# Optimization experiments

Measured on AMD Instinct MI355X. Metric: run time of the kernel, lower is better.

## Reference

```python
import jax, jax.numpy as jnp
import numpy as np

B, S, D, H, DH, DK = 2, 2048, 1024, 16, 64, 64


def setup_inputs() -> dict:
    key = jax.random.key(0)
    ks = jax.random.split(key, 11)
    scale_in = 1.0 / np.sqrt(D)
    return {
        "Q": jax.random.normal(ks[0], (B, S, D), jnp.float32),
        "K": jax.random.normal(ks[1], (B, S, D), jnp.float32),
        "V": jax.random.normal(ks[2], (B, S, D), jnp.float32),
        "Wq": jax.random.normal(ks[3], (H, D, DH), jnp.float32) * scale_in,
        "bq": jax.random.normal(ks[4], (H, DH), jnp.float32) * 0.02,
        "Wk": jax.random.normal(ks[5], (H, D, DH), jnp.float32) * scale_in,
        "bk": jax.random.normal(ks[6], (H, DH), jnp.float32) * 0.02,
        "Wv": jax.random.normal(ks[7], (H, D, DH), jnp.float32) * scale_in,
        "bv": jax.random.normal(ks[8], (H, DH), jnp.float32) * 0.02,
        "Wf": jax.random.normal(ks[9], (D, D), jnp.float32) * scale_in,
        "bf": jax.random.normal(ks[10], (D,), jnp.float32) * 0.02,
    }


def reference(Q, K, V, Wq, bq, Wk, bk, Wv, bv, Wf, bf):
    # Per-head projections, vectorized over the head axis h. [B,H,S,DH]
    Qh = jnp.einsum("bsd,hde->bhse", Q, Wq) + bq[None, :, None, :]
    Kh = jnp.einsum("bsd,hde->bhse", K, Wk) + bk[None, :, None, :]
    Vh = jnp.einsum("bsd,hde->bhse", V, Wv) + bv[None, :, None, :]
    inv_sqrt_dk = jnp.asarray(1.0 / np.sqrt(DK), Qh.dtype)
    # Full attention matrix [B,H,S,S] (faithful to the naive original).
    scores = jnp.einsum("bhse,bhte->bhst", Qh, Kh) * inv_sqrt_dk
    attn = jax.nn.softmax(scores, axis=-1)  # F.softmax default -> last dim
    out = jnp.einsum("bhst,bhte->bhse", attn, Vh)  # [B,H,S,DH]
    # Concat heads on the feature axis: [B,S,H*DH] == [B,S,D]
    out = out.transpose(0, 2, 1, 3).reshape(Q.shape[0], Q.shape[1], -1)
    return out @ Wf + bf
```

## Files before the change

### kernel.cpp

```cpp
#include <hip/hip_runtime.h>

#define DEV __device__ __forceinline__

typedef unsigned short u16;
typedef unsigned int   u32;
typedef __attribute__((ext_vector_type(4)))  float f32x4;
typedef __attribute__((ext_vector_type(8)))  short s16x8;
typedef __attribute__((ext_vector_type(2)))  u32   u32x2;

static constexpr size_t OFF_QBF  = 0;
static constexpr size_t OFF_KBF  = 8388608;
static constexpr size_t OFF_VBF  = 16777216;
static constexpr size_t OFF_WCAT = 25165824;
static constexpr size_t OFF_WFT  = 31457280;
static constexpr size_t OFF_BIAS = 33554432;
static constexpr size_t OFF_QKVH = 33566720;
static constexpr size_t OFF_VT   = 58732544;
static constexpr size_t OFF_OBUF = 67121152;

DEV u16 f2bf(float f) {
  union { float f; u32 u; } a; a.f = f;
  u32 r = a.u + 0x7FFFu + ((a.u >> 16) & 1u);
  return (u16)(r >> 16);
}
DEV u32 f2bf2(float lo, float hi_) {
  return (u32)f2bf(lo) | ((u32)f2bf(hi_) << 16);
}

#if __has_builtin(__builtin_amdgcn_exp2f)
DEV float fast_exp2(float x) { return __builtin_amdgcn_exp2f(x); }
#else
DEV float fast_exp2(float x) { return exp2f(x); }
#endif

DEV f32x4 mfma16(s16x8 a, s16x8 b, f32x4 c) {
  return __builtin_amdgcn_mfma_f32_16x16x32_bf16(a, b, c, 0, 0, 0);
}

DEV void gload_lds16(const void* g, void* l) {
  __builtin_amdgcn_global_load_lds(
      (__attribute__((address_space(1))) void*)g,
      (__attribute__((address_space(3))) void*)l, 16, 0, 0);
}

__global__ __launch_bounds__(256) void prep_all_k(const float* __restrict__ Q,
                                                  const float* __restrict__ K,
                                                  const float* __restrict__ V,
                                                  const float* __restrict__ Wq,
                                                  const float* __restrict__ Wk,
                                                  const float* __restrict__ Wv,
                                                  const float* __restrict__ Wf,
                                                  const float* __restrict__ bq,
                                                  const float* __restrict__ bk,
                                                  const float* __restrict__ bv,
                                                  u16* __restrict__ QKVbf,
                                                  u16* __restrict__ Wcat,
                                                  u16* __restrict__ WfT,
                                                  float* __restrict__ biascat) {
  const int bid = blockIdx.x;
  __shared__ u16 t[64][72];
  if (bid < 12288) {
    size_t idx = (size_t)bid * 256 + threadIdx.x;
    size_t tt  = idx >> 20;
    size_t r   = idx & 1048575;
    const float* src = (tt == 0) ? Q : (tt == 1) ? K : V;
    f32x4 v = *(const f32x4*)(src + r * 4);
    u32x2 o;
    o[0] = f2bf2(v[0], v[1]);
    o[1] = f2bf2(v[2], v[3]);
    *(u32x2*)(QKVbf + idx * 4) = o;
  } else if (bid < 13056) {
    const int q = bid - 12288;
    const int dt = q & 15, h = (q >> 4) & 15, z = q >> 8;
    const float* W = (z == 0) ? Wq : (z == 1) ? Wk : Wv;
#pragma unroll
    for (int p = 0; p < 16; ++p) {
      int idx = threadIdx.x + p * 256;
      int r = idx >> 6, e = idx & 63;
      t[r][e] = f2bf(W[((size_t)h * 1024 + dt * 64 + r) * 64 + e]);
    }
    __syncthreads();
#pragma unroll
    for (int p = 0; p < 16; ++p) {
      int idx = threadIdx.x + p * 256;
      int e = idx >> 6, r = idx & 63;
      Wcat[((size_t)z * 1024 + h * 64 + e) * 1024 + dt * 64 + r] = t[r][e];
    }
  } else if (bid < 13312) {
    const int q = bid - 13056;
    const int dt = q & 15, ft = q >> 4;
#pragma unroll
    for (int p = 0; p < 16; ++p) {
      int idx = threadIdx.x + p * 256;
      int r = idx >> 6, f = idx & 63;
      t[r][f] = f2bf(Wf[(size_t)(dt * 64 + r) * 1024 + ft * 64 + f]);
    }
    __syncthreads();
#pragma unroll
    for (int p = 0; p < 16; ++p) {
      int idx = threadIdx.x + p * 256;
      int f = idx >> 6, r = idx & 63;
      WfT[(size_t)(ft * 64 + f) * 1024 + dt * 64 + r] = t[r][f];
    }
  } else {
    int i = (bid - 13312) * 256 + threadIdx.x;
    if (i < 1024) biascat[i] = bq[i];
    else if (i < 2048) biascat[i] = bk[i - 1024];
    else if (i < 3072) biascat[i] = bv[i - 2048];
  }
}

template <int MODE>
DEV void gemm128(const u16* __restrict__ A, int lda,
                 const u16* __restrict__ B, int ldb,
                 const float* __restrict__ bias,
                 void* __restrict__ Cp, size_t ldc, int K) {
  __shared__ u16 Ash[128 * 32];
  __shared__ u16 Bsh[128 * 32];
  const int tid = threadIdx.x;
  const int lane = tid & 63;
  const int w = tid >> 6;
  const int wr = w >> 1, wc = w & 1;
  const int lr = lane >> 2;
  const int lc = (lane & 3) << 3;
  const int l15 = lane & 15, lg = lane >> 4;

  f32x4 acc[4][4];
#pragma unroll
  for (int i = 0; i < 4; ++i)
#pragma unroll
    for (int j = 0; j < 4; ++j) acc[i][j] = f32x4{0.f, 0.f, 0.f, 0.f};

  for (int kt = 0; kt < K; kt += 32) {
    if (kt) __syncthreads();
#pragma unroll
    for (int j = 0; j < 2; ++j) {
      const u16* ga = A + (size_t)(w * 32 + j * 16 + lr) * lda + kt + lc;
      gload_lds16(ga, (char*)Ash + (w * 2 + j) * 1024);
      const u16* gb = B + (size_t)(w * 32 + j * 16 + lr) * ldb + kt + lc;
      gload_lds16(gb, (char*)Bsh + (w * 2 + j) * 1024);
    }
    __syncthreads();
    s16x8 af[4], bv_[4];
#pragma unroll
    for (int i = 0; i < 4; ++i) {
      af[i]  = *(const s16x8*)&Ash[(wr * 64 + i * 16 + l15) * 32 + lg * 8];
      bv_[i] = *(const s16x8*)&Bsh[(wc * 64 + i * 16 + l15) * 32 + lg * 8];
    }
#pragma unroll
    for (int mf = 0; mf < 4; ++mf)
#pragma unroll
      for (int nf = 0; nf < 4; ++nf)
        acc[mf][nf] = mfma16(af[mf], bv_[nf], acc[mf][nf]);
  }
#pragma unroll
  for (int nf = 0; nf < 4; ++nf) {
    const int nn = wc * 64 + nf * 16 + l15;
    const float bvv = bias[nn];
#pragma unroll
    for (int mf = 0; mf < 4; ++mf) {
      if (MODE == 2) {
        const int mm0 = wr * 64 + mf * 16 + lg * 4;
        u32x2 d;
        d[0] = f2bf2(acc[mf][nf][0] + bvv, acc[mf][nf][1] + bvv);
        d[1] = f2bf2(acc[mf][nf][2] + bvv, acc[mf][nf][3] + bvv);
        *(u32x2*)((u16*)Cp + (size_t)nn * ldc + mm0) = d;
      } else {
#pragma unroll
        for (int j = 0; j < 4; ++j) {
          const int mm = wr * 64 + mf * 16 + lg * 4 + j;
          float v = acc[mf][nf][j] + bvv;
          if (MODE == 1) ((u16*)Cp)[(size_t)mm * ldc + nn] = f2bf(v);
          else           ((float*)Cp)[(size_t)mm * ldc + nn] = v;
        }
      }
    }
  }
}

__global__ __launch_bounds__(256) void proj_gemm_k(const u16* __restrict__ Qb,
                                                   const u16* __restrict__ Kb,
                                                   const u16* __restrict__ Vb,
                                                   const u16* __restrict__ Wcat,
                                                   const float* __restrict__ biascat,
                                                   u16* __restrict__ QKVh,
                                                   u16* __restrict__ Vt) {
  const int z = blockIdx.z;
  const u16* A = (z == 0) ? Qb : (z == 1) ? Kb : Vb;
  const int m0 = blockIdx.y * 128;
  const int nl = blockIdx.x * 128;
  if (z == 2) {
    gemm128<2>(A + (size_t)m0 * 1024, 1024,
               Wcat + (size_t)(2 * 1024 + nl) * 1024, 1024,
               biascat + 2 * 1024 + nl,
               Vt + (size_t)nl * 4096 + m0, 4096, 1024);
  } else {
    gemm128<1>(A + (size_t)m0 * 1024, 1024,
               Wcat + (size_t)(z * 1024 + nl) * 1024, 1024,
               biascat + z * 1024 + nl,
               QKVh + (size_t)m0 * 3072 + z * 1024 + nl, 3072, 1024);
  }
}

__global__ __launch_bounds__(256) void final_gemm_k(const u16* __restrict__ Obuf,
                                                    const u16* __restrict__ WfT,
                                                    const float* __restrict__ bf,
                                                    float* __restrict__ out) {
  const int m0 = blockIdx.y * 128;
  const int n0 = blockIdx.x * 128;
  gemm128<0>(Obuf + (size_t)m0 * 1024, 1024,
             WfT + (size_t)n0 * 1024, 1024,
             bf + n0,
             out + (size_t)m0 * 1024 + n0, 1024, 1024);
}

__global__ __launch_bounds__(512) void attn8_k(const u16* __restrict__ QKVh,
                                               const u16* __restrict__ Vt,
                                               u16* __restrict__ Obuf) {
  const int id = blockIdx.x;
  const int virt = (id & 7) * 64 + (id >> 3);
  const int qb = virt & 15;
  const int hb = virt >> 4;
  const int h = hb & 15, b = hb >> 4;

  const int tid = threadIdx.x, lane = tid & 63, w = tid >> 6;
  const int l15 = lane & 15, lg = lane >> 4;

  __shared__ u16 Ksh[64 * 64];
  __shared__ u16 Vsh[64 * 64];
  __shared__ u16 Psh[8][16 * 64];

  const size_t rowQ = (size_t)(b * 2048 + qb * 128);
  const u16* Qbase = QKVh + rowQ * 3072 + h * 64;
  const u16* Kbase = QKVh + (size_t)(b * 2048) * 3072 + 1024 + h * 64;
  const u16* Vbase = Vt + (size_t)(h * 64) * 4096 + b * 2048;

  s16x8 aq[2];
#pragma unroll
  for (int kf = 0; kf < 2; ++kf)
    aq[kf] = *(const s16x8*)(Qbase + (size_t)(w * 16 + l15) * 3072 + kf * 32 + lg * 8);

  f32x4 accO[4];
  f32x4 lacc = f32x4{0.f, 0.f, 0.f, 0.f};
#pragma unroll
  for (int nf = 0; nf < 4; ++nf) accO[nf] = f32x4{0.f, 0.f, 0.f, 0.f};

  const float CSC = 0.18033688011112042f;
  const float M2 = 12.0f;
  const s16x8 ONESV = {0x3F80, 0x3F80, 0x3F80, 0x3F80,
                       0x3F80, 0x3F80, 0x3F80, 0x3F80};

  const int sr = tid >> 3, ch = tid & 7;
  const int sswz = (sr & 7) << 4;
  const u16* Kg = Kbase + (size_t)sr * 3072 + ch * 8;
  const u16* Vg = Vbase + (size_t)sr * 4096 + ch * 8;

  s16x8 kreg = *(const s16x8*)Kg;
  s16x8 vreg = *(const s16x8*)Vg;
  Kg += (size_t)64 * 3072;
  Vg += 64;

  for (int kt = 0; kt < 32; ++kt) {
    if (kt) __syncthreads();
    *(s16x8*)((char*)Ksh + sr * 128 + ((ch * 16) ^ sswz)) = kreg;
    *(s16x8*)((char*)Vsh + sr * 128 + ((ch * 16) ^ sswz)) = vreg;
    __syncthreads();

    if (kt < 31) {
      kreg = *(const s16x8*)Kg;
      vreg = *(const s16x8*)Vg;
      Kg += (size_t)64 * 3072;
      Vg += 64;
    }

    f32x4 sc[4];
#pragma unroll
    for (int nf = 0; nf < 4; ++nf) sc[nf] = f32x4{0.f, 0.f, 0.f, 0.f};
#pragma unroll
    for (int kf = 0; kf < 2; ++kf) {
      s16x8 kb[4];
#pragma unroll
      for (int nf = 0; nf < 4; ++nf) {
        int row = nf * 16 + l15;
        kb[nf] = *(const s16x8*)((char*)Ksh + row * 128 + ((kf * 64 + lg * 16) ^ ((row & 7) << 4)));
      }
#pragma unroll
      for (int nf = 0; nf < 4; ++nf)
        sc[nf] = mfma16(aq[kf], kb[nf], sc[nf]);
    }

#pragma unroll
    for (int nf = 0; nf < 4; ++nf)
#pragma unroll
      for (int j = 0; j < 4; ++j)
        sc[nf][j] = fast_exp2(fmaf(sc[nf][j], CSC, -M2));

    char* pbase = (char*)&Psh[w][0];
#pragma unroll
    for (int nf = 0; nf < 4; ++nf)
#pragma unroll
      for (int j = 0; j < 4; ++j) {
        int srow = lg * 4 + j;
        int tcol = nf * 16 + l15;
        *(u16*)(pbase + srow * 128 + ((tcol * 2) ^ ((srow & 7) << 4))) =
            f2bf(sc[nf][j]);
      }
    asm volatile("s_waitcnt lgkmcnt(0)" ::: "memory");
    __builtin_amdgcn_sched_barrier(0);

#pragma unroll
    for (int kf = 0; kf < 2; ++kf) {
      s16x8 pa, vb[4];
      pa = *(const s16x8*)(pbase + l15 * 128 + ((kf * 64 + lg * 16) ^ ((l15 & 7) << 4)));
#pragma unroll
      for (int nf = 0; nf < 4; ++nf) {
        int row = nf * 16 + l15;
        vb[nf] = *(const s16x8*)((char*)Vsh + row * 128 + ((kf * 64 + lg * 16) ^ ((row & 7) << 4)));
      }
#pragma unroll
      for (int nf = 0; nf < 4; ++nf)
        accO[nf] = mfma16(pa, vb[nf], accO[nf]);
      lacc = mfma16(pa, ONESV, lacc);
    }
  }

  u16* Ob = Obuf + rowQ * 1024 + h * 64;
  float inv[4];
#pragma unroll
  for (int j = 0; j < 4; ++j) inv[j] = 1.f / lacc[j];
#pragma unroll
  for (int nf = 0; nf < 4; ++nf)
#pragma unroll
    for (int j = 0; j < 4; ++j)
      Ob[(size_t)(w * 16 + lg * 4 + j) * 1024 + nf * 16 + l15] =
          f2bf(accO[nf][j] * inv[j]);
}

extern "C" void kernel_launch(void* const* d_in, const int* in_sizes, int n_in,
                              void* d_out, int out_size, void* d_ws, size_t ws_size,
                              hipStream_t stream) {
  const float* Q  = (const float*)d_in[0];
  const float* K  = (const float*)d_in[1];
  const float* V  = (const float*)d_in[2];
  const float* Wq = (const float*)d_in[3];
  const float* bq = (const float*)d_in[4];
  const float* Wk = (const float*)d_in[5];
  const float* bk = (const float*)d_in[6];
  const float* Wv = (const float*)d_in[7];
  const float* bv = (const float*)d_in[8];
  const float* Wf = (const float*)d_in[9];
  const float* bf = (const float*)d_in[10];
  float* out = (float*)d_out;
  char* ws = (char*)d_ws;

  u16*   QKVbf  = (u16*)(ws + OFF_QBF);
  u16*   Qbf    = (u16*)(ws + OFF_QBF);
  u16*   Kbf    = (u16*)(ws + OFF_KBF);
  u16*   Vbf    = (u16*)(ws + OFF_VBF);
  u16*   Wcat   = (u16*)(ws + OFF_WCAT);
  u16*   WfT    = (u16*)(ws + OFF_WFT);
  float* biascat= (float*)(ws + OFF_BIAS);
  u16*   QKVh   = (u16*)(ws + OFF_QKVH);
  u16*   Vt     = (u16*)(ws + OFF_VT);
  u16*   Obuf   = (u16*)(ws + OFF_OBUF);

  dim3 blk(256);
  prep_all_k<<<13324, blk, 0, stream>>>(Q, K, V, Wq, Wk, Wv, Wf, bq, bk, bv,
                                        QKVbf, Wcat, WfT, biascat);
  proj_gemm_k<<<dim3(8, 32, 3), blk, 0, stream>>>(Qbf, Kbf, Vbf, Wcat, biascat,
                                                  QKVh, Vt);
  attn8_k<<<dim3(512), dim3(512), 0, stream>>>(QKVh, Vt, Obuf);
  final_gemm_k<<<dim3(8, 32), blk, 0, stream>>>(Obuf, WfT, bf, out);
}
```

Measured before the change: 137.0 us.

## Rewrite attention kernel with 32x32 MFMA tiles, four waves, and LDS-staged output

The attention kernel changes from 16x16x32 MFMA with eight waves of 16 query rows to 32x32x16 MFMA with four waves of 32 query rows each. It computes S^T (K as A-operand) so the softmax row sum is a register reduction plus one shuffle, replacing the extra ones-vector MFMA. P is written to LDS as packed 8-byte stores, and the output is staged through LDS for coalesced 16-byte global writes. Fewer waves per block lowers latency hiding, and the larger accumulators raise register pressure.

```diff
diff --git a/kernel.cpp b/kernel.cpp
--- a/kernel.cpp
+++ b/kernel.cpp
@@ -5,6 +5,7 @@
 typedef unsigned short u16;
 typedef unsigned int   u32;
 typedef __attribute__((ext_vector_type(4)))  float f32x4;
+typedef __attribute__((ext_vector_type(16))) float f32x16;
 typedef __attribute__((ext_vector_type(8)))  short s16x8;
 typedef __attribute__((ext_vector_type(2)))  u32   u32x2;
 
@@ -35,6 +36,9 @@
 
 DEV f32x4 mfma16(s16x8 a, s16x8 b, f32x4 c) {
   return __builtin_amdgcn_mfma_f32_16x16x32_bf16(a, b, c, 0, 0, 0);
+}
+DEV f32x16 mfma32(s16x8 a, s16x8 b, f32x16 c) {
+  return __builtin_amdgcn_mfma_f32_32x32x16_bf16(a, b, c, 0, 0, 0);
 }
 
 DEV void gload_lds16(const void* g, void* l) {
@@ -214,9 +218,9 @@
              out + (size_t)m0 * 1024 + n0, 1024, 1024);
 }
 
-__global__ __launch_bounds__(512) void attn8_k(const u16* __restrict__ QKVh,
-                                               const u16* __restrict__ Vt,
-                                               u16* __restrict__ Obuf) {
+__global__ __launch_bounds__(256) void attn10_k(const u16* __restrict__ QKVh,
+                                                const u16* __restrict__ Vt,
+                                                u16* __restrict__ Obuf) {
   const int id = blockIdx.x;
   const int virt = (id & 7) * 64 + (id >> 3);
   const int qb = virt & 15;
@@ -224,116 +228,133 @@
   const int h = hb & 15, b = hb >> 4;
 
   const int tid = threadIdx.x, lane = tid & 63, w = tid >> 6;
-  const int l15 = lane & 15, lg = lane >> 4;
-
-  __shared__ u16 Ksh[64 * 64];
-  __shared__ u16 Vsh[64 * 64];
-  __shared__ u16 Psh[8][16 * 64];
+  const int l31 = lane & 31, hi = lane >> 5;
+  const int swz = (l31 & 7) << 4;
+
+  __shared__ u16 KVsh[2][64 * 64];
+  __shared__ u16 Psh[4][32 * 64];
 
   const size_t rowQ = (size_t)(b * 2048 + qb * 128);
   const u16* Qbase = QKVh + rowQ * 3072 + h * 64;
   const u16* Kbase = QKVh + (size_t)(b * 2048) * 3072 + 1024 + h * 64;
   const u16* Vbase = Vt + (size_t)(h * 64) * 4096 + b * 2048;
 
-  s16x8 aq[2];
-#pragma unroll
-  for (int kf = 0; kf < 2; ++kf)
-    aq[kf] = *(const s16x8*)(Qbase + (size_t)(w * 16 + l15) * 3072 + kf * 32 + lg * 8);
-
-  f32x4 accO[4];
-  f32x4 lacc = f32x4{0.f, 0.f, 0.f, 0.f};
-#pragma unroll
-  for (int nf = 0; nf < 4; ++nf) accO[nf] = f32x4{0.f, 0.f, 0.f, 0.f};
+  s16x8 qf[4];
+#pragma unroll
+  for (int ks = 0; ks < 4; ++ks)
+    qf[ks] = *(const s16x8*)(Qbase + (size_t)(w * 32 + l31) * 3072 + ks * 16 + hi * 8);
+
+  f32x16 accO0, accO1;
+#pragma unroll
+  for (int i = 0; i < 16; ++i) { accO0[i] = 0.f; accO1[i] = 0.f; }
+  float lrun = 0.f;
 
   const float CSC = 0.18033688011112042f;
   const float M2 = 12.0f;
-  const s16x8 ONESV = {0x3F80, 0x3F80, 0x3F80, 0x3F80,
-                       0x3F80, 0x3F80, 0x3F80, 0x3F80};
 
   const int sr = tid >> 3, ch = tid & 7;
   const int sswz = (sr & 7) << 4;
   const u16* Kg = Kbase + (size_t)sr * 3072 + ch * 8;
   const u16* Vg = Vbase + (size_t)sr * 4096 + ch * 8;
 
-  s16x8 kreg = *(const s16x8*)Kg;
-  s16x8 vreg = *(const s16x8*)Vg;
+  s16x8 kreg0 = *(const s16x8*)Kg;
+  s16x8 kreg1 = *(const s16x8*)(Kg + (size_t)32 * 3072);
+  s16x8 vreg0 = *(const s16x8*)Vg;
+  s16x8 vreg1 = *(const s16x8*)(Vg + (size_t)32 * 4096);
   Kg += (size_t)64 * 3072;
   Vg += 64;
 
+  char* const kb = (char*)&KVsh[0][0];
+  char* const vb = (char*)&KVsh[1][0];
+  char* const pbase = (char*)&Psh[w][0];
+
   for (int kt = 0; kt < 32; ++kt) {
     if (kt) __syncthreads();
-    *(s16x8*)((char*)Ksh + sr * 128 + ((ch * 16) ^ sswz)) = kreg;
-    *(s16x8*)((char*)Vsh + sr * 128 + ((ch * 16) ^ sswz)) = vreg;
+    *(s16x8*)(kb + sr * 128 + ((ch * 16) ^ sswz)) = kreg0;
+    *(s16x8*)(kb + (sr + 32) * 128 + ((ch * 16) ^ sswz)) = kreg1;
+    *(s16x8*)(vb + sr * 128 + ((ch * 16) ^ sswz)) = vreg0;
+    *(s16x8*)(vb + (sr + 32) * 128 + ((ch * 16) ^ sswz)) = vreg1;
     __syncthreads();
 
     if (kt < 31) {
-      kreg = *(const s16x8*)Kg;
-      vreg = *(const s16x8*)Vg;
+      kreg0 = *(const s16x8*)Kg;
+      kreg1 = *(const s16x8*)(Kg + (size_t)32 * 3072);
+      vreg0 = *(const s16x8*)Vg;
+      vreg1 = *(const s16x8*)(Vg + (size_t)32 * 4096);
       Kg += (size_t)64 * 3072;
       Vg += 64;
     }
 
-    f32x4 sc[4];
-#pragma unroll
-    for (int nf = 0; nf < 4; ++nf) sc[nf] = f32x4{0.f, 0.f, 0.f, 0.f};
-#pragma unroll
-    for (int kf = 0; kf < 2; ++kf) {
-      s16x8 kb[4];
-#pragma unroll
-      for (int nf = 0; nf < 4; ++nf) {
-        int row = nf * 16 + l15;
-        kb[nf] = *(const s16x8*)((char*)Ksh + row * 128 + ((kf * 64 + lg * 16) ^ ((row & 7) << 4)));
-      }
-#pragma unroll
-      for (int nf = 0; nf < 4; ++nf)
-        sc[nf] = mfma16(aq[kf], kb[nf], sc[nf]);
-    }
-
-#pragma unroll
-    for (int nf = 0; nf < 4; ++nf)
-#pragma unroll
-      for (int j = 0; j < 4; ++j)
-        sc[nf][j] = fast_exp2(fmaf(sc[nf][j], CSC, -M2));
-
-    char* pbase = (char*)&Psh[w][0];
-#pragma unroll
-    for (int nf = 0; nf < 4; ++nf)
-#pragma unroll
-      for (int j = 0; j < 4; ++j) {
-        int srow = lg * 4 + j;
-        int tcol = nf * 16 + l15;
-        *(u16*)(pbase + srow * 128 + ((tcol * 2) ^ ((srow & 7) << 4))) =
-            f2bf(sc[nf][j]);
-      }
+    f32x16 sc0, sc1;
+#pragma unroll
+    for (int i = 0; i < 16; ++i) { sc0[i] = 0.f; sc1[i] = 0.f; }
+#pragma unroll
+    for (int ks = 0; ks < 4; ++ks) {
+      s16x8 ka0 = *(const s16x8*)(kb + l31 * 128 + ((ks * 32 + hi * 16) ^ swz));
+      s16x8 ka1 = *(const s16x8*)(kb + (32 + l31) * 128 + ((ks * 32 + hi * 16) ^ swz));
+      sc0 = mfma32(ka0, qf[ks], sc0);
+      sc1 = mfma32(ka1, qf[ks], sc1);
+    }
+
+    float ls = 0.f;
+#pragma unroll
+    for (int i = 0; i < 16; ++i) {
+      sc0[i] = fast_exp2(fmaf(sc0[i], CSC, -M2));
+      ls += sc0[i];
+    }
+#pragma unroll
+    for (int i = 0; i < 16; ++i) {
+      sc1[i] = fast_exp2(fmaf(sc1[i], CSC, -M2));
+      ls += sc1[i];
+    }
+    lrun += ls + __shfl_xor(ls, 32);
+
+#pragma unroll
+    for (int q = 0; q < 4; ++q) {
+      u32x2 d0, d1;
+      d0[0] = f2bf2(sc0[4 * q + 0], sc0[4 * q + 1]);
+      d0[1] = f2bf2(sc0[4 * q + 2], sc0[4 * q + 3]);
+      *(u32x2*)(pbase + l31 * 128 + ((q * 16 + hi * 8) ^ swz)) = d0;
+      d1[0] = f2bf2(sc1[4 * q + 0], sc1[4 * q + 1]);
+      d1[1] = f2bf2(sc1[4 * q + 2], sc1[4 * q + 3]);
+      *(u32x2*)(pbase + l31 * 128 + ((64 + q * 16 + hi * 8) ^ swz)) = d1;
+    }
     asm volatile("s_waitcnt lgkmcnt(0)" ::: "memory");
     __builtin_amdgcn_sched_barrier(0);
 
 #pragma unroll
-    for (int kf = 0; kf < 2; ++kf) {
-      s16x8 pa, vb[4];
-      pa = *(const s16x8*)(pbase + l15 * 128 + ((kf * 64 + lg * 16) ^ ((l15 & 7) << 4)));
-#pragma unroll
-      for (int nf = 0; nf < 4; ++nf) {
-        int row = nf * 16 + l15;
-        vb[nf] = *(const s16x8*)((char*)Vsh + row * 128 + ((kf * 64 + lg * 16) ^ ((row & 7) << 4)));
-      }
-#pragma unroll
-      for (int nf = 0; nf < 4; ++nf)
-        accO[nf] = mfma16(pa, vb[nf], accO[nf]);
-      lacc = mfma16(pa, ONESV, lacc);
-    }
-  }
-
-  u16* Ob = Obuf + rowQ * 1024 + h * 64;
-  float inv[4];
-#pragma unroll
-  for (int j = 0; j < 4; ++j) inv[j] = 1.f / lacc[j];
-#pragma unroll
-  for (int nf = 0; nf < 4; ++nf)
-#pragma unroll
-    for (int j = 0; j < 4; ++j)
-      Ob[(size_t)(w * 16 + lg * 4 + j) * 1024 + nf * 16 + l15] =
-          f2bf(accO[nf][j] * inv[j]);
+    for (int ks = 0; ks < 4; ++ks) {
+      s16x8 pb  = *(const s16x8*)(pbase + l31 * 128 + ((ks * 32 + hi * 16) ^ swz));
+      s16x8 va0 = *(const s16x8*)(vb + l31 * 128 + ((ks * 32 + hi * 16) ^ swz));
+      s16x8 va1 = *(const s16x8*)(vb + (32 + l31) * 128 + ((ks * 32 + hi * 16) ^ swz));
+      accO0 = mfma32(va0, pb, accO0);
+      accO1 = mfma32(va1, pb, accO1);
+    }
+  }
+
+  __syncthreads();
+  const float inv = 1.f / lrun;
+  char* osh = kb + w * 4096;
+#pragma unroll
+  for (int q = 0; q < 4; ++q) {
+    u32x2 d0, d1;
+    d0[0] = f2bf2(accO0[4 * q + 0] * inv, accO0[4 * q + 1] * inv);
+    d0[1] = f2bf2(accO0[4 * q + 2] * inv, accO0[4 * q + 3] * inv);
+    *(u32x2*)(osh + l31 * 128 + ((q * 16 + hi * 8) ^ swz)) = d0;
+    d1[0] = f2bf2(accO1[4 * q + 0] * inv, accO1[4 * q + 1] * inv);
+    d1[1] = f2bf2(accO1[4 * q + 2] * inv, accO1[4 * q + 3] * inv);
+    *(u32x2*)(osh + l31 * 128 + ((64 + q * 16 + hi * 8) ^ swz)) = d1;
+  }
+  asm volatile("s_waitcnt lgkmcnt(0)" ::: "memory");
+  __builtin_amdgcn_sched_barrier(0);
+  u16* Ob = Obuf + (rowQ + w * 32) * 1024 + h * 64;
+#pragma unroll
+  for (int c = 0; c < 4; ++c) {
+    int idx = lane + c * 64;
+    int row = idx >> 3, cc = idx & 7;
+    s16x8 v = *(const s16x8*)(osh + row * 128 + ((cc * 16) ^ ((row & 7) << 4)));
+    *(s16x8*)(Ob + (size_t)row * 1024 + cc * 8) = v;
+  }
 }
 
 extern "C" void kernel_launch(void* const* d_in, const int* in_sizes, int n_in,
@@ -369,6 +390,6 @@
                                         QKVbf, Wcat, WfT, biascat);
   proj_gemm_k<<<dim3(8, 32, 3), blk, 0, stream>>>(Qbf, Kbf, Vbf, Wcat, biascat,
                                                   QKVh, Vt);
-  attn8_k<<<dim3(512), dim3(512), 0, stream>>>(QKVh, Vt, Obuf);
+  attn10_k<<<dim3(512), blk, 0, stream>>>(QKVh, Vt, Obuf);
   final_gemm_k<<<dim3(8, 32), blk, 0, stream>>>(Obuf, WfT, bf, out);
 }
```

New measurement: 141.9 us. 1.04x slower.
